# Kernel tuning notes

Measured on AMD Instinct MI355X. Metric: run time of the kernel, lower is better.

The kernel has to match this reference:

```python
import math
import jax, jax.numpy as jnp
import numpy as np

B, S, D, L = 8, 4096, 1024, 16

def setup_inputs() -> dict:
    key = jax.random.key(0)
    k1, k2, k3 = jax.random.split(key, 3)
    memory = jax.random.normal(k1, (B, S, D), dtype=jnp.float32)
    summarizer = jax.random.normal(k2, (L, D), dtype=jnp.float32) * 0.02
    w_proj = jax.random.normal(k3, (1, L), dtype=jnp.float32) * (1.0 / math.sqrt(L))
    return {"memory": memory, "summarizer": summarizer, "w_proj": w_proj}

def reference(memory, summarizer, w_proj):
    # scores: [B, L, S] = summarizer @ memory^T / sqrt(D)
    d = summarizer.shape[-1]
    scores = jnp.einsum('ld,bsd->bls', summarizer, memory) / jnp.sqrt(jnp.asarray(d, memory.dtype))
    p_attn = jax.nn.softmax(scores, axis=-1)            # softmax over sequence S
    ctx = jnp.einsum('bls,bsd->bld', p_attn, memory)    # [B, L, D]
    # nn.Linear(L, 1, bias=False) applied to ctx.transpose(-1,-2): [B, D, L] @ W^T -> [B, D, 1]
    out = jnp.einsum('bld,l->bd', ctx, w_proj[0])       # [B, D]
    return out[:, None, :]                              # [B, 1, D] after final transpose
```

## Files before the change

### kernel.cpp

```cpp
#include <hip/hip_runtime.h>

#define SS 4096
#define DD 1024
#define LL 16
#define ROWF 1028

typedef __attribute__((ext_vector_type(8))) short short8;
typedef __attribute__((ext_vector_type(4))) float fl4;

static __device__ __forceinline__ short f2bf(float f) {
    unsigned u = __float_as_uint(f);
    u += 0x7FFFu + ((u >> 16) & 1u);
    return (short)(u >> 16);
}

static __device__ __forceinline__ short8 pack8(fl4 a, fl4 b) {
    short8 r;
    r[0] = f2bf(a[0]); r[1] = f2bf(a[1]); r[2] = f2bf(a[2]); r[3] = f2bf(a[3]);
    r[4] = f2bf(b[0]); r[5] = f2bf(b[1]); r[6] = f2bf(b[2]); r[7] = f2bf(b[3]);
    return r;
}

static __device__ __forceinline__ void dma16(const float* g, float* l) {
    __builtin_amdgcn_global_load_lds(
        (const __attribute__((address_space(1))) void*)g,
        (__attribute__((address_space(3))) void*)l, 16, 0, 0);
}

__global__ __launch_bounds__(512) void k_main(const float* __restrict__ mem,
                                              const float* __restrict__ summ,
                                              float* __restrict__ part,
                                              float* __restrict__ Zpart) {
    __shared__ float buf[2][8 * ROWF];
    __shared__ float e_lds[8 * LL];
    __shared__ float scr[8][256];

    int blk = blockIdx.x;
    int b   = blk >> 6;
    int s_base = (blk & 63) << 6;
    int t    = threadIdx.x;
    int wv   = t >> 6;
    int lane = t & 63;
    int o  = lane & 15;
    int qd = lane >> 4;

    const float* gseg = mem + ((size_t)b * SS + s_base) * DD;

    fl4 a0[4], a1[4];
    {
        const float* arow = summ + o * DD + wv * 128 + qd * 8;
        #pragma unroll
        for (int j = 0; j < 4; ++j) {
            a0[j] = *(const fl4*)(arow + j * 32);
            a1[j] = *(const fl4*)(arow + j * 32 + 4);
        }
    }
    short8 afr[4];
    #pragma unroll
    for (int j = 0; j < 4; ++j) afr[j] = pack8(a0[j], a1[j]);

    #pragma unroll
    for (int c = 0; c < 4; ++c)
        dma16(gseg + (size_t)wv * DD + c * 256 + lane * 4,
              &buf[0][wv * ROWF + c * 256]);

    int lg = t >> 8;
    int q  = t & 255;
    int s_sm = t & 7;
    int l_sm = (t >> 3) & 15;
    int scr_idx = ((l_sm >> 2) * 16 + s_sm) * 4 + (l_sm & 3);

    fl4 ctx[8];
    #pragma unroll
    for (int l = 0; l < 8; ++l) ctx[l] = (fl4){0.f, 0.f, 0.f, 0.f};
    float z = 0.f;
    const float scale = 0.03125f;

    for (int g = 0; g < 8; ++g) {
        if (g > 0) {
            const float* mrow = &buf[(g - 1) & 1][0] + q * 4;
            const fl4* erow = (const fl4*)&e_lds[lg * 8];
            #pragma unroll
            for (int s = 0; s < 8; ++s) {
                fl4 m4 = *(const fl4*)(mrow + s * ROWF);
                fl4 e0 = erow[s * 4];
                fl4 e1 = erow[s * 4 + 1];
                #pragma unroll
                for (int j = 0; j < 4; ++j) {
                    ctx[j]     += e0[j] * m4;
                    ctx[4 + j] += e1[j] * m4;
                }
            }
        }
        asm volatile("s_waitcnt lgkmcnt(0)" ::: "memory");
        __builtin_amdgcn_sched_barrier(0);
        __builtin_amdgcn_s_barrier();
        __builtin_amdgcn_sched_barrier(0);

        if (g < 7) {
            const float* gp = gseg + (size_t)(g + 1) * 8 * DD;
            float* nb = &buf[(g + 1) & 1][wv * ROWF];
            dma16(gp + (size_t)wv * DD +   0 + lane * 4, nb +   0);
            dma16(gp + (size_t)wv * DD + 256 + lane * 4, nb + 256);
            dma16(gp + (size_t)wv * DD + 512 + lane * 4, nb + 512);
            dma16(gp + (size_t)wv * DD + 768 + lane * 4, nb + 768);
            asm volatile("s_waitcnt vmcnt(4)" ::: "memory");
        } else {
            asm volatile("s_waitcnt vmcnt(0)" ::: "memory");
        }
        __builtin_amdgcn_sched_barrier(0);
        __builtin_amdgcn_s_barrier();
        __builtin_amdgcn_sched_barrier(0);

        const float* bbase = &buf[g & 1][0];
        fl4 acc = {0.f, 0.f, 0.f, 0.f};
        const float* brow = bbase + (o & 7) * ROWF + wv * 128 + qd * 8;
        #pragma unroll
        for (int j = 0; j < 4; ++j) {
            fl4 f0 = *(const fl4*)(brow + j * 32);
            fl4 f1 = *(const fl4*)(brow + j * 32 + 4);
            acc = __builtin_amdgcn_mfma_f32_16x16x32_bf16(afr[j], pack8(f0, f1),
                                                          acc, 0, 0, 0);
        }
        *(fl4*)&scr[wv][lane * 4] = acc;
        asm volatile("s_waitcnt lgkmcnt(0)" ::: "memory");
        __builtin_amdgcn_s_barrier();
        __builtin_amdgcn_sched_barrier(0);

        if (t < 128) {
            float sum = 0.f;
            #pragma unroll
            for (int w8 = 0; w8 < 8; ++w8) sum += scr[w8][scr_idx];
            float ev = __expf(sum * scale);
            e_lds[s_sm * LL + l_sm] = ev;
            z += ev;
        }
        asm volatile("s_waitcnt lgkmcnt(0)" ::: "memory");
        __builtin_amdgcn_s_barrier();
        __builtin_amdgcn_sched_barrier(0);
    }

    {
        const float* mrow = &buf[7 & 1][0] + q * 4;
        const fl4* erow = (const fl4*)&e_lds[lg * 8];
        #pragma unroll
        for (int s = 0; s < 8; ++s) {
            fl4 m4 = *(const fl4*)(mrow + s * ROWF);
            fl4 e0 = erow[s * 4];
            fl4 e1 = erow[s * 4 + 1];
            #pragma unroll
            for (int j = 0; j < 4; ++j) {
                ctx[j]     += e0[j] * m4;
                ctx[4 + j] += e1[j] * m4;
            }
        }
    }

    float* pp = part + (size_t)blk * LL * DD + (size_t)(lg * 8) * DD + q * 4;
    #pragma unroll
    for (int l = 0; l < 8; ++l) *(fl4*)(pp + (size_t)l * DD) = ctx[l];

    if (t < 128) {
        float v = z;
        v += __shfl_xor(v, 1, 64);
        v += __shfl_xor(v, 2, 64);
        v += __shfl_xor(v, 4, 64);
        if (s_sm == 0) Zpart[blk * LL + l_sm] = v;
    }
}

__global__ __launch_bounds__(256) void k_out(const float* __restrict__ part,
                                             const float* __restrict__ Zpart,
                                             const float* __restrict__ w,
                                             float* __restrict__ out) {
    int blkid = blockIdx.x;
    int b  = blkid >> 5;
    int d0 = (blkid & 31) << 5;
    int t = threadIdx.x;
    __shared__ float coef[LL];
    __shared__ fl4 red[32][8];

    if (t < LL) {
        float Z = 0.f;
        #pragma unroll
        for (int s = 0; s < 64; ++s) Z += Zpart[(b * 64 + s) * LL + t];
        coef[t] = w[t] / Z;
    }
    __syncthreads();

    int dq = t & 7;
    int sg = t >> 3;
    fl4 acc = {0.f, 0.f, 0.f, 0.f};
    #pragma unroll
    for (int h = 0; h < 2; ++h) {
        const float* pb = part + (size_t)(b * 64 + sg + h * 32) * LL * DD + d0 + dq * 4;
        #pragma unroll
        for (int l = 0; l < LL; ++l) {
            fl4 v = *(const fl4*)(pb + (size_t)l * DD);
            acc += coef[l] * v;
        }
    }
    red[sg][dq] = acc;
    __syncthreads();

    if (t < 8) {
        fl4 s = {0.f, 0.f, 0.f, 0.f};
        #pragma unroll
        for (int g = 0; g < 32; ++g) s += red[g][t];
        *(fl4*)&out[b * DD + d0 + t * 4] = s;
    }
}

extern "C" void kernel_launch(void* const* d_in, const int* in_sizes, int n_in,
                              void* d_out, int out_size, void* d_ws, size_t ws_size,
                              hipStream_t stream) {
    const float* mem  = (const float*)d_in[0];
    const float* summ = (const float*)d_in[1];
    const float* w    = (const float*)d_in[2];
    float* out = (float*)d_out;

    char* ws = (char*)d_ws;
    float* Zpart = (float*)ws;
    float* part  = (float*)(ws + 64 * 1024);

    k_main<<<512, 512, 0, stream>>>(mem, summ, part, Zpart);
    k_out<<<256, 256, 0, stream>>>(part, Zpart, w, out);
}
```

Measured before the change: 209.3 us.

## Drop LDS staging of memory tiles; read global directly with 16-row chunks

Removes the double-buffered global_load_lds staging of memory rows into LDS and instead has each wave read memory directly from global, both for the MFMA score computation and for the context accumulation. The loop is restructured into 4 chunks of 16 sequence rows with a full 16-wide MFMA tile, halving per-chunk barriers, and each thread now owns 2 columns for all 16 summarizer rows. This cuts LDS traffic and capacity but reads each memory row twice from global/L2 (once for scores, once for context) and loses the explicit async prefetch overlap.

Measured after the change: 216.6 us. 3.5% more time.

```diff
diff --git a/kernel.cpp b/kernel.cpp
--- a/kernel.cpp
+++ b/kernel.cpp
@@ -3,10 +3,10 @@
 #define SS 4096
 #define DD 1024
 #define LL 16
-#define ROWF 1028
 
 typedef __attribute__((ext_vector_type(8))) short short8;
 typedef __attribute__((ext_vector_type(4))) float fl4;
+typedef __attribute__((ext_vector_type(2))) float fl2;
 
 static __device__ __forceinline__ short f2bf(float f) {
     unsigned u = __float_as_uint(f);
@@ -21,100 +21,45 @@
     return r;
 }
 
-static __device__ __forceinline__ void dma16(const float* g, float* l) {
-    __builtin_amdgcn_global_load_lds(
-        (const __attribute__((address_space(1))) void*)g,
-        (__attribute__((address_space(3))) void*)l, 16, 0, 0);
-}
-
 __global__ __launch_bounds__(512) void k_main(const float* __restrict__ mem,
                                               const float* __restrict__ summ,
                                               float* __restrict__ part,
                                               float* __restrict__ Zpart) {
-    __shared__ float buf[2][8 * ROWF];
-    __shared__ float e_lds[8 * LL];
-    __shared__ float scr[8][256];
+    __shared__ float scr[2][8][256];
+    __shared__ float e_lds[2][16][LL];
 
     int blk = blockIdx.x;
     int b   = blk >> 6;
-    int s_base = (blk & 63) << 6;
+    int s0  = (blk & 63) << 6;
     int t    = threadIdx.x;
     int wv   = t >> 6;
     int lane = t & 63;
     int o  = lane & 15;
     int qd = lane >> 4;
 
-    const float* gseg = mem + ((size_t)b * SS + s_base) * DD;
-
-    fl4 a0[4], a1[4];
+    short8 afr[4];
     {
         const float* arow = summ + o * DD + wv * 128 + qd * 8;
         #pragma unroll
         for (int j = 0; j < 4; ++j) {
-            a0[j] = *(const fl4*)(arow + j * 32);
-            a1[j] = *(const fl4*)(arow + j * 32 + 4);
+            fl4 a0 = *(const fl4*)(arow + j * 32);
+            fl4 a1 = *(const fl4*)(arow + j * 32 + 4);
+            afr[j] = pack8(a0, a1);
         }
     }
-    short8 afr[4];
+
+    fl2 ctx[LL];
     #pragma unroll
-    for (int j = 0; j < 4; ++j) afr[j] = pack8(a0[j], a1[j]);
-
-    #pragma unroll
-    for (int c = 0; c < 4; ++c)
-        dma16(gseg + (size_t)wv * DD + c * 256 + lane * 4,
-              &buf[0][wv * ROWF + c * 256]);
-
-    int lg = t >> 8;
-    int q  = t & 255;
-    int s_sm = t & 7;
-    int l_sm = (t >> 3) & 15;
-    int scr_idx = ((l_sm >> 2) * 16 + s_sm) * 4 + (l_sm & 3);
-
-    fl4 ctx[8];
-    #pragma unroll
-    for (int l = 0; l < 8; ++l) ctx[l] = (fl4){0.f, 0.f, 0.f, 0.f};
-    float z = 0.f;
+    for (int l = 0; l < LL; ++l) ctx[l] = (fl2){0.f, 0.f};
+    fl4 zacc = {0.f, 0.f, 0.f, 0.f};
     const float scale = 0.03125f;
 
-    for (int g = 0; g < 8; ++g) {
-        if (g > 0) {
-            const float* mrow = &buf[(g - 1) & 1][0] + q * 4;
-            const fl4* erow = (const fl4*)&e_lds[lg * 8];
-            #pragma unroll
-            for (int s = 0; s < 8; ++s) {
-                fl4 m4 = *(const fl4*)(mrow + s * ROWF);
-                fl4 e0 = erow[s * 4];
-                fl4 e1 = erow[s * 4 + 1];
-                #pragma unroll
-                for (int j = 0; j < 4; ++j) {
-                    ctx[j]     += e0[j] * m4;
-                    ctx[4 + j] += e1[j] * m4;
-                }
-            }
-        }
-        asm volatile("s_waitcnt lgkmcnt(0)" ::: "memory");
-        __builtin_amdgcn_sched_barrier(0);
-        __builtin_amdgcn_s_barrier();
-        __builtin_amdgcn_sched_barrier(0);
+    const float* gb = mem + ((size_t)b * SS + s0) * DD;
 
-        if (g < 7) {
-            const float* gp = gseg + (size_t)(g + 1) * 8 * DD;
-            float* nb = &buf[(g + 1) & 1][wv * ROWF];
-            dma16(gp + (size_t)wv * DD +   0 + lane * 4, nb +   0);
-            dma16(gp + (size_t)wv * DD + 256 + lane * 4, nb + 256);
-            dma16(gp + (size_t)wv * DD + 512 + lane * 4, nb + 512);
-            dma16(gp + (size_t)wv * DD + 768 + lane * 4, nb + 768);
-            asm volatile("s_waitcnt vmcnt(4)" ::: "memory");
-        } else {
-            asm volatile("s_waitcnt vmcnt(0)" ::: "memory");
-        }
-        __builtin_amdgcn_sched_barrier(0);
-        __builtin_amdgcn_s_barrier();
-        __builtin_amdgcn_sched_barrier(0);
-
-        const float* bbase = &buf[g & 1][0];
+    #pragma unroll 2
+    for (int c = 0; c < 4; ++c) {
+        const float* brow = gb + (size_t)(c * 16 + o) * DD + wv * 128 + qd * 8;
         fl4 acc = {0.f, 0.f, 0.f, 0.f};
-        const float* brow = bbase + (o & 7) * ROWF + wv * 128 + qd * 8;
         #pragma unroll
         for (int j = 0; j < 4; ++j) {
             fl4 f0 = *(const fl4*)(brow + j * 32);
@@ -122,50 +67,56 @@
             acc = __builtin_amdgcn_mfma_f32_16x16x32_bf16(afr[j], pack8(f0, f1),
                                                           acc, 0, 0, 0);
         }
-        *(fl4*)&scr[wv][lane * 4] = acc;
+        *(fl4*)&scr[c & 1][wv][lane * 4] = acc;
         asm volatile("s_waitcnt lgkmcnt(0)" ::: "memory");
         __builtin_amdgcn_s_barrier();
         __builtin_amdgcn_sched_barrier(0);
 
-        if (t < 128) {
-            float sum = 0.f;
+        if (wv == 0) {
+            fl4 sum = {0.f, 0.f, 0.f, 0.f};
             #pragma unroll
-            for (int w8 = 0; w8 < 8; ++w8) sum += scr[w8][scr_idx];
-            float ev = __expf(sum * scale);
-            e_lds[s_sm * LL + l_sm] = ev;
-            z += ev;
+            for (int w8 = 0; w8 < 8; ++w8)
+                sum += *(const fl4*)&scr[c & 1][w8][lane * 4];
+            fl4 ev;
+            #pragma unroll
+            for (int r = 0; r < 4; ++r) ev[r] = __expf(sum[r] * scale);
+            *(fl4*)&e_lds[c & 1][o][qd * 4] = ev;
+            zacc += ev;
         }
         asm volatile("s_waitcnt lgkmcnt(0)" ::: "memory");
         __builtin_amdgcn_s_barrier();
         __builtin_amdgcn_sched_barrier(0);
-    }
 
-    {
-        const float* mrow = &buf[7 & 1][0] + q * 4;
-        const fl4* erow = (const fl4*)&e_lds[lg * 8];
-        #pragma unroll
-        for (int s = 0; s < 8; ++s) {
-            fl4 m4 = *(const fl4*)(mrow + s * ROWF);
-            fl4 e0 = erow[s * 4];
-            fl4 e1 = erow[s * 4 + 1];
+        const float* mrow = gb + (size_t)(c * 16) * DD + wv * 128 + lane * 2;
+        #pragma unroll 4
+        for (int s = 0; s < 16; ++s) {
+            fl2 m2 = *(const fl2*)(mrow + (size_t)s * DD);
             #pragma unroll
-            for (int j = 0; j < 4; ++j) {
-                ctx[j]     += e0[j] * m4;
-                ctx[4 + j] += e1[j] * m4;
+            for (int g4 = 0; g4 < 4; ++g4) {
+                fl4 e4 = *(const fl4*)&e_lds[c & 1][s][g4 * 4];
+                ctx[g4 * 4 + 0] += e4[0] * m2;
+                ctx[g4 * 4 + 1] += e4[1] * m2;
+                ctx[g4 * 4 + 2] += e4[2] * m2;
+                ctx[g4 * 4 + 3] += e4[3] * m2;
             }
         }
     }
 
-    float* pp = part + (size_t)blk * LL * DD + (size_t)(lg * 8) * DD + q * 4;
+    float* pp = part + (size_t)blk * LL * DD + wv * 128 + lane * 2;
     #pragma unroll
-    for (int l = 0; l < 8; ++l) *(fl4*)(pp + (size_t)l * DD) = ctx[l];
+    for (int l = 0; l < LL; ++l) *(fl2*)(pp + (size_t)l * DD) = ctx[l];
 
-    if (t < 128) {
-        float v = z;
-        v += __shfl_xor(v, 1, 64);
-        v += __shfl_xor(v, 2, 64);
-        v += __shfl_xor(v, 4, 64);
-        if (s_sm == 0) Zpart[blk * LL + l_sm] = v;
+    if (wv == 0) {
+        #pragma unroll
+        for (int r = 0; r < 4; ++r) {
+            float v = zacc[r];
+            v += __shfl_xor(v, 1, 64);
+            v += __shfl_xor(v, 2, 64);
+            v += __shfl_xor(v, 4, 64);
+            v += __shfl_xor(v, 8, 64);
+            zacc[r] = v;
+        }
+        if (o == 0) *(fl4*)&Zpart[blk * LL + qd * 4] = zacc;
     }
 }
 
```
